# Kernel tuning notes

Measured on AMD Instinct MI355X. Metric: run time of the kernel, lower is better.

## Reference

```python
import jax, jax.numpy as jnp
import numpy as np

N = 50000
IN_CH = 256
HID = 256
E = 800000


def setup_inputs() -> dict:
    key = jax.random.key(0)
    ks = jax.random.split(key, 12)
    s = 1.0 / np.sqrt(HID)
    return {
        "x": jax.random.normal(ks[0], (N, IN_CH), jnp.float32),
        "edge_index": jax.random.randint(ks[1], (2, E), 0, N, dtype=jnp.int64),
        "prev_embedding": jax.random.normal(ks[2], (N, HID), jnp.float32),
        "W1": jax.random.normal(ks[3], (IN_CH, HID), jnp.float32) / np.sqrt(IN_CH),
        "b1": jnp.zeros((HID,), jnp.float32),
        "W2": jax.random.normal(ks[4], (HID, HID), jnp.float32) * s,
        "b2": jnp.zeros((HID,), jnp.float32),
        "gWw": jax.random.normal(ks[5], (HID, HID), jnp.float32) * s,
        "gWb": jnp.zeros((HID,), jnp.float32),
        "gUw": jax.random.normal(ks[6], (HID, HID), jnp.float32) * s,
        "gUb": jnp.zeros((HID,), jnp.float32),
    }


def _gcn_conv(x, W, b, src, dst, norm):
    # PyG GCNConv: h = x @ W; out[i] = sum_j norm_ij * h[j]; + bias
    h = x @ W
    msg = h[src] * norm[:, None]  # [E+N, H]
    out = jax.ops.segment_sum(msg, dst, num_segments=N)
    return out + b


def _norm_and_loops(edge_index):
    loop = jnp.arange(N, dtype=edge_index.dtype)
    src = jnp.concatenate([edge_index[0], loop])
    dst = jnp.concatenate([edge_index[1], loop])
    deg = jax.ops.segment_sum(jnp.ones_like(dst, dtype=jnp.float32), dst, num_segments=N)
    dinv = jnp.where(deg > 0, jax.lax.rsqrt(deg), 0.0)
    norm = dinv[src] * dinv[dst]
    return src, dst, norm


def reference(x, edge_index, prev_embedding, W1, b1, W2, b2, gWw, gWb, gUw, gUb):
    src, dst, norm = _norm_and_loops(edge_index)
    h = jax.nn.relu(_gcn_conv(x, W1, b1, src, dst, norm))
    h_t = _gcn_conv(h, W2, b2, src, dst, norm)
    alpha = jax.nn.sigmoid(h_t @ gWw + gWb + prev_embedding @ gUw + gUb)
    h_tilde = alpha * h_t + (1.0 - alpha) * prev_embedding
    return (h_tilde, h_t)
```

## Files before the change

### kernel.cpp

```cpp
#include <hip/hip_runtime.h>
#include <hip/hip_bf16.h>
#include <math.h>

#define HIDC 256
#define LSTR 40

typedef short short8 __attribute__((ext_vector_type(8)));
typedef float f32x4 __attribute__((ext_vector_type(4)));

__device__ __forceinline__ ushort f2bf_rne(float f) {
    uint u = __float_as_uint(f);
    u += 0x7FFF + ((u >> 16) & 1);
    return (ushort)(u >> 16);
}
__device__ __forceinline__ float bf2f(ushort h) {
    return __uint_as_float(((uint)h) << 16);
}


__global__ void fill_i_kernel(int* __restrict__ p, int v, int n) {
    int i = blockIdx.x * 256 + threadIdx.x;
    if (i < n) p[i] = v;
}

__global__ void deg_kernel(const int* __restrict__ dst, int* __restrict__ deg, int E) {
    int e = blockIdx.x * 256 + threadIdx.x;
    if (e < E) atomicAdd(&deg[dst[e]], 1);
}


__device__ __forceinline__ int block_incl_scan(int v, int tid) {
#pragma unroll
    for (int off = 1; off < 64; off <<= 1) {
        int t = __shfl_up(v, off);
        if ((tid & 63) >= off) v += t;
    }
    __shared__ int wt[4];
    if ((tid & 63) == 63) wt[tid >> 6] = v;
    __syncthreads();
    int wid = tid >> 6;
    for (int w = 0; w < wid; w++) v += wt[w];
    __syncthreads();
    return v;
}

__global__ void scan_a_kernel(const int* __restrict__ deg, int* __restrict__ row_start,
                              int* __restrict__ blocksum, float* __restrict__ dinv, int N) {
    int tid = threadIdx.x;
    int i = blockIdx.x * 256 + tid;
    int v = (i < N) ? deg[i] : 0;
    int incl = block_incl_scan(v, tid);
    if (i < N) {
        row_start[i + 1] = incl;
        dinv[i] = rsqrtf((float)(v + 1));
    }
    if (tid == 255) blocksum[blockIdx.x] = incl;
}

__global__ void scan_b_kernel(int* __restrict__ blocksum, int nb) {
    int tid = threadIdx.x;
    int v = (tid < nb) ? blocksum[tid] : 0;
    int incl = block_incl_scan(v, tid);
    if (tid < nb) blocksum[tid] = incl;
}

__global__ void scan_c_kernel(int* __restrict__ row_start, int* __restrict__ cursor,
                              const int* __restrict__ blocksum, int N) {
    int b = blockIdx.x;
    int i = b * 256 + threadIdx.x;
    int add = (b > 0) ? blocksum[b - 1] : 0;
    if (i < N) {
        int v = row_start[i + 1] + add;
        row_start[i + 1] = v;
        cursor[i + 1] = v;
    }
    if (b == 0 && threadIdx.x == 0) { row_start[0] = 0; cursor[0] = 0; }
}

__global__ void scatter_kernel(const int* __restrict__ src, const int* __restrict__ dst,
                               const float* __restrict__ dinv, int* __restrict__ cursor,
                               int* __restrict__ csr_src, float* __restrict__ csr_w, int E) {
    int e = blockIdx.x * 256 + threadIdx.x;
    if (e < E) {
        int s = src[e], d = dst[e];
        int pos = atomicAdd(&cursor[d], 1);
        csr_src[pos] = s;
        csr_w[pos] = dinv[s] * dinv[d];
    }
}


__global__ void prep_all_kernel(const float* __restrict__ W1, const float* __restrict__ W2,
                                const float* __restrict__ gWw, const float* __restrict__ gUw,
                                ushort* __restrict__ Bt1, ushort* __restrict__ Bt2,
                                ushort* __restrict__ Bth, ushort* __restrict__ Btl) {
    int n = blockIdx.x, k = threadIdx.x;
    Bt1[n * 256 + k] = f2bf_rne(W1[k * 256 + n]);
    Bt2[n * 256 + k] = f2bf_rne(W2[k * 256 + n]);
    float v1 = gWw[k * 256 + n];
    uint u1 = __float_as_uint(v1);
    Bth[n * 512 + k] = (ushort)(u1 >> 16);
    Btl[n * 512 + k] = f2bf_rne(v1 - __uint_as_float(u1 & 0xFFFF0000u));
    float v2 = gUw[k * 256 + n];
    uint u2 = __float_as_uint(v2);
    Bth[n * 512 + 256 + k] = (ushort)(u2 >> 16);
    Btl[n * 512 + 256 + k] = f2bf_rne(v2 - __uint_as_float(u2 & 0xFFFF0000u));
}


__global__ __launch_bounds__(256, 4) void gemm_bf16_kernel(
    const float* __restrict__ A, const ushort* __restrict__ Bt,
    ushort* __restrict__ C, int M)
{
    __shared__ __align__(16) ushort As[128 * LSTR];
    __shared__ __align__(16) ushort Bs[128 * LSTR];
    const int tl = threadIdx.x;
    const int lane = tl & 63, wave = tl >> 6;
    const int wm = (wave & 1) * 64, wn = (wave >> 1) * 64;
    const int bm = blockIdx.x * 128, bn = blockIdx.y * 128;

    const int ar  = tl >> 1;
    const int akq = (tl & 1) * 16;
    const bool aok = (bm + ar) < M;

    f32x4 acc[4][4] = {};

    for (int k0 = 0; k0 < 256; k0 += 32) {
        {
            const float* ap = A + (size_t)(bm + ar) * HIDC + k0 + akq;
#pragma unroll
            for (int j = 0; j < 4; j++) {
                float4 v = aok ? *(const float4*)(ap + 4 * j) : make_float4(0.f, 0.f, 0.f, 0.f);
                ushort4 h;
                h.x = f2bf_rne(v.x); h.y = f2bf_rne(v.y);
                h.z = f2bf_rne(v.z); h.w = f2bf_rne(v.w);
                *(ushort4*)&As[ar * LSTR + akq + 4 * j] = h;
            }
        }
        {
            const ushort* bp = Bt + (size_t)(bn + ar) * 256 + k0 + akq;
            *(uint4*)&Bs[ar * LSTR + akq]     = *(const uint4*)bp;
            *(uint4*)&Bs[ar * LSTR + akq + 8] = *(const uint4*)(bp + 8);
        }
        __syncthreads();
        const int fr = lane & 15, koff = (lane >> 4) * 8;
        short8 af[4], bfv[4];
#pragma unroll
        for (int t = 0; t < 4; t++) {
            af[t]  = *(const short8*)&As[(wm + t * 16 + fr) * LSTR + koff];
            bfv[t] = *(const short8*)&Bs[(wn + t * 16 + fr) * LSTR + koff];
        }
#pragma unroll
        for (int mt = 0; mt < 4; mt++)
#pragma unroll
            for (int nt = 0; nt < 4; nt++)
                acc[mt][nt] = __builtin_amdgcn_mfma_f32_16x16x32_bf16(af[mt], bfv[nt], acc[mt][nt], 0, 0, 0);
        __syncthreads();
    }

    const int row4 = (lane >> 4) * 4, coln = lane & 15;
#pragma unroll
    for (int mt = 0; mt < 4; mt++)
#pragma unroll
        for (int r = 0; r < 4; r++) {
            int m = bm + wm + mt * 16 + row4 + r;
            if (m < M) {
#pragma unroll
                for (int nt = 0; nt < 4; nt++) {
                    int n = bn + wn + nt * 16 + coln;
                    C[(size_t)m * HIDC + n] = f2bf_rne(acc[mt][nt][r]);
                }
            }
        }
}


__global__ __launch_bounds__(256, 4) void gemm_bf16A_kernel(
    const ushort* __restrict__ A, const ushort* __restrict__ Bt,
    ushort* __restrict__ C, int M)
{
    __shared__ __align__(16) ushort As[128 * LSTR];
    __shared__ __align__(16) ushort Bs[128 * LSTR];
    const int tl = threadIdx.x;
    const int lane = tl & 63, wave = tl >> 6;
    const int wm = (wave & 1) * 64, wn = (wave >> 1) * 64;
    const int bm = blockIdx.x * 128, bn = blockIdx.y * 128;

    const int ar  = tl >> 1;
    const int akq = (tl & 1) * 16;
    const bool aok = (bm + ar) < M;

    f32x4 acc[4][4] = {};

    for (int k0 = 0; k0 < 256; k0 += 32) {
        {
            const ushort* ap = A + (size_t)(bm + ar) * HIDC + k0 + akq;
            uint4 z = make_uint4(0u, 0u, 0u, 0u);
            *(uint4*)&As[ar * LSTR + akq]     = aok ? *(const uint4*)ap       : z;
            *(uint4*)&As[ar * LSTR + akq + 8] = aok ? *(const uint4*)(ap + 8) : z;
        }
        {
            const ushort* bp = Bt + (size_t)(bn + ar) * 256 + k0 + akq;
            *(uint4*)&Bs[ar * LSTR + akq]     = *(const uint4*)bp;
            *(uint4*)&Bs[ar * LSTR + akq + 8] = *(const uint4*)(bp + 8);
        }
        __syncthreads();
        const int fr = lane & 15, koff = (lane >> 4) * 8;
        short8 af[4], bfv[4];
#pragma unroll
        for (int t = 0; t < 4; t++) {
            af[t]  = *(const short8*)&As[(wm + t * 16 + fr) * LSTR + koff];
            bfv[t] = *(const short8*)&Bs[(wn + t * 16 + fr) * LSTR + koff];
        }
#pragma unroll
        for (int mt = 0; mt < 4; mt++)
#pragma unroll
            for (int nt = 0; nt < 4; nt++)
                acc[mt][nt] = __builtin_amdgcn_mfma_f32_16x16x32_bf16(af[mt], bfv[nt], acc[mt][nt], 0, 0, 0);
        __syncthreads();
    }

    const int row4 = (lane >> 4) * 4, coln = lane & 15;
#pragma unroll
    for (int mt = 0; mt < 4; mt++)
#pragma unroll
        for (int r = 0; r < 4; r++) {
            int m = bm + wm + mt * 16 + row4 + r;
            if (m < M) {
#pragma unroll
                for (int nt = 0; nt < 4; nt++) {
                    int n = bn + wn + nt * 16 + coln;
                    C[(size_t)m * HIDC + n] = f2bf_rne(acc[mt][nt][r]);
                }
            }
        }
}


__global__ __launch_bounds__(256, 4) void gate_kernel(
    const float* __restrict__ ht, const float* __restrict__ prev,
    const ushort* __restrict__ Bth, const ushort* __restrict__ Btl,
    const float* __restrict__ gWb, const float* __restrict__ gUb,
    float* __restrict__ out, int M)
{
    __shared__ __align__(16) ushort Ash[64 * LSTR];
    __shared__ __align__(16) ushort Asl[64 * LSTR];
    __shared__ __align__(16) ushort Bsh[128 * LSTR];
    __shared__ __align__(16) ushort Bsl[128 * LSTR];
    const int tl = threadIdx.x;
    const int lane = tl & 63, wave = tl >> 6;
    const int wm = (wave & 1) * 32, wn = (wave >> 1) * 64;
    const int bm = blockIdx.x * 64, bn = blockIdx.y * 128;

    const int arA = tl >> 2;
    const int kqA = (tl & 3) * 8;
    const int arB = tl >> 1;
    const int kqB = (tl & 1) * 16;
    const bool aok = (bm + arA) < M;

    f32x4 acc[2][4] = {};

    for (int k0 = 0; k0 < 512; k0 += 32) {
        {
            const float* srcA = (k0 < 256) ? ht : prev;
            const float* ap = srcA + (size_t)(bm + arA) * HIDC + (k0 & 255) + kqA;
            float4 v0 = aok ? *(const float4*)(ap)     : make_float4(0.f, 0.f, 0.f, 0.f);
            float4 v1 = aok ? *(const float4*)(ap + 4) : make_float4(0.f, 0.f, 0.f, 0.f);
            float vv[8] = {v0.x, v0.y, v0.z, v0.w, v1.x, v1.y, v1.z, v1.w};
            ushort hp[8], lp[8];
#pragma unroll
            for (int q = 0; q < 8; q++) {
                uint u = __float_as_uint(vv[q]);
                hp[q] = (ushort)(u >> 16);
                lp[q] = f2bf_rne(vv[q] - __uint_as_float(u & 0xFFFF0000u));
            }
            *(ushort4*)&Ash[arA * LSTR + kqA]     = make_ushort4(hp[0], hp[1], hp[2], hp[3]);
            *(ushort4*)&Ash[arA * LSTR + kqA + 4] = make_ushort4(hp[4], hp[5], hp[6], hp[7]);
            *(ushort4*)&Asl[arA * LSTR + kqA]     = make_ushort4(lp[0], lp[1], lp[2], lp[3]);
            *(ushort4*)&Asl[arA * LSTR + kqA + 4] = make_ushort4(lp[4], lp[5], lp[6], lp[7]);
        }
        {
            const ushort* bph = Bth + (size_t)(bn + arB) * 512 + k0 + kqB;
            const ushort* bpl = Btl + (size_t)(bn + arB) * 512 + k0 + kqB;
            *(uint4*)&Bsh[arB * LSTR + kqB]     = *(const uint4*)bph;
            *(uint4*)&Bsh[arB * LSTR + kqB + 8] = *(const uint4*)(bph + 8);
            *(uint4*)&Bsl[arB * LSTR + kqB]     = *(const uint4*)bpl;
            *(uint4*)&Bsl[arB * LSTR + kqB + 8] = *(const uint4*)(bpl + 8);
        }
        __syncthreads();
        const int fr = lane & 15, koff = (lane >> 4) * 8;
        short8 afh[2], afl[2], bfh[4], bfl[4];
#pragma unroll
        for (int t = 0; t < 2; t++) {
            afh[t] = *(const short8*)&Ash[(wm + t * 16 + fr) * LSTR + koff];
            afl[t] = *(const short8*)&Asl[(wm + t * 16 + fr) * LSTR + koff];
        }
#pragma unroll
        for (int t = 0; t < 4; t++) {
            bfh[t] = *(const short8*)&Bsh[(wn + t * 16 + fr) * LSTR + koff];
            bfl[t] = *(const short8*)&Bsl[(wn + t * 16 + fr) * LSTR + koff];
        }
#pragma unroll
        for (int mt = 0; mt < 2; mt++)
#pragma unroll
            for (int nt = 0; nt < 4; nt++) {
                acc[mt][nt] = __builtin_amdgcn_mfma_f32_16x16x32_bf16(afh[mt], bfh[nt], acc[mt][nt], 0, 0, 0);
                acc[mt][nt] = __builtin_amdgcn_mfma_f32_16x16x32_bf16(afh[mt], bfl[nt], acc[mt][nt], 0, 0, 0);
                acc[mt][nt] = __builtin_amdgcn_mfma_f32_16x16x32_bf16(afl[mt], bfh[nt], acc[mt][nt], 0, 0, 0);
            }
        __syncthreads();
    }

    const int row4 = (lane >> 4) * 4, coln = lane & 15;
#pragma unroll
    for (int mt = 0; mt < 2; mt++)
#pragma unroll
        for (int r = 0; r < 4; r++) {
            int m = bm + wm + mt * 16 + row4 + r;
            if (m < M) {
#pragma unroll
                for (int nt = 0; nt < 4; nt++) {
                    int n = bn + wn + nt * 16 + coln;
                    size_t idx = (size_t)m * HIDC + n;
                    float g = acc[mt][nt][r] + gWb[n] + gUb[n];
                    float alpha = 1.f / (1.f + expf(-g));
                    out[idx] = alpha * ht[idx] + (1.f - alpha) * prev[idx];
                }
            }
        }
}


__global__ __launch_bounds__(256) void csr_agg_kernel(
    const ushort* __restrict__ hm, const int* __restrict__ row_start,
    const int* __restrict__ csr_src, const float* __restrict__ csr_w,
    const float* __restrict__ dinv, const float* __restrict__ bias,
    float* __restrict__ outf, ushort* __restrict__ outb, int do_relu, int N)
{
    const int wave = threadIdx.x >> 6, lane = threadIdx.x & 63;
    const int i = blockIdx.x * 4 + wave;
    if (i >= N) return;
    const int c = lane * 4;

    const float di = dinv[i];
    const float s2 = di * di;
    ushort4 sv = *(const ushort4*)(hm + (size_t)i * HIDC + c);
    float a0 = s2 * bf2f(sv.x), a1 = s2 * bf2f(sv.y);
    float a2 = s2 * bf2f(sv.z), a3 = s2 * bf2f(sv.w);

    const int b0 = row_start[i], b1 = row_start[i + 1];
    int t = b0;
    for (; t + 8 <= b1; t += 8) {
        int   ix[8]; float wv[8]; ushort4 vv[8];
#pragma unroll
        for (int q = 0; q < 8; q++) { ix[q] = csr_src[t + q]; wv[q] = csr_w[t + q]; }
#pragma unroll
        for (int q = 0; q < 8; q++) vv[q] = *(const ushort4*)(hm + (size_t)ix[q] * HIDC + c);
#pragma unroll
        for (int q = 0; q < 8; q++) {
            a0 += wv[q] * bf2f(vv[q].x); a1 += wv[q] * bf2f(vv[q].y);
            a2 += wv[q] * bf2f(vv[q].z); a3 += wv[q] * bf2f(vv[q].w);
        }
    }
    for (; t + 4 <= b1; t += 4) {
        int   i0 = csr_src[t],     i1 = csr_src[t + 1];
        int   i2 = csr_src[t + 2], i3 = csr_src[t + 3];
        float w0 = csr_w[t],       w1 = csr_w[t + 1];
        float w2 = csr_w[t + 2],   w3 = csr_w[t + 3];
        ushort4 v0 = *(const ushort4*)(hm + (size_t)i0 * HIDC + c);
        ushort4 v1 = *(const ushort4*)(hm + (size_t)i1 * HIDC + c);
        ushort4 v2 = *(const ushort4*)(hm + (size_t)i2 * HIDC + c);
        ushort4 v3 = *(const ushort4*)(hm + (size_t)i3 * HIDC + c);
        a0 += w0 * bf2f(v0.x); a1 += w0 * bf2f(v0.y); a2 += w0 * bf2f(v0.z); a3 += w0 * bf2f(v0.w);
        a0 += w1 * bf2f(v1.x); a1 += w1 * bf2f(v1.y); a2 += w1 * bf2f(v1.z); a3 += w1 * bf2f(v1.w);
        a0 += w2 * bf2f(v2.x); a1 += w2 * bf2f(v2.y); a2 += w2 * bf2f(v2.z); a3 += w2 * bf2f(v2.w);
        a0 += w3 * bf2f(v3.x); a1 += w3 * bf2f(v3.y); a2 += w3 * bf2f(v3.z); a3 += w3 * bf2f(v3.w);
    }
    for (; t < b1; ++t) {
        int s_ = csr_src[t];
        float w = csr_w[t];
        ushort4 v = *(const ushort4*)(hm + (size_t)s_ * HIDC + c);
        a0 += w * bf2f(v.x); a1 += w * bf2f(v.y); a2 += w * bf2f(v.z); a3 += w * bf2f(v.w);
    }

    float4 bb = *(const float4*)(bias + c);
    a0 += bb.x; a1 += bb.y; a2 += bb.z; a3 += bb.w;
    if (do_relu) {
        a0 = fmaxf(a0, 0.f); a1 = fmaxf(a1, 0.f);
        a2 = fmaxf(a2, 0.f); a3 = fmaxf(a3, 0.f);
    }
    if (outb) {
        ushort4 o;
        o.x = f2bf_rne(a0); o.y = f2bf_rne(a1);
        o.z = f2bf_rne(a2); o.w = f2bf_rne(a3);
        *(ushort4*)(outb + (size_t)i * HIDC + c) = o;
    } else {
        *(float4*)(outf + (size_t)i * HIDC + c) = make_float4(a0, a1, a2, a3);
    }
}


extern "C" void kernel_launch(void* const* d_in, const int* in_sizes, int n_in,
                              void* d_out, int out_size, void* d_ws, size_t ws_size,
                              hipStream_t stream) {
    const float* x    = (const float*)d_in[0];
    const int*   ei   = (const int*)d_in[1];
    const float* prev = (const float*)d_in[2];
    const float* W1   = (const float*)d_in[3];
    const float* b1   = (const float*)d_in[4];
    const float* W2   = (const float*)d_in[5];
    const float* b2   = (const float*)d_in[6];
    const float* gWw  = (const float*)d_in[7];
    const float* gWb  = (const float*)d_in[8];
    const float* gUw  = (const float*)d_in[9];
    const float* gUb  = (const float*)d_in[10];

    const int N = in_sizes[0] / HIDC;
    const int E = in_sizes[1] / 2;
    const int* src = ei;
    const int* dst = ei + E;

    float* out  = (float*)d_out;
    float* out1 = out;
    float* ht   = out + (size_t)N * HIDC;
    ushort* hbf = (ushort*)out1;

    float* ws = (float*)d_ws;
    size_t o = 0;
    auto take = [&](size_t n) { size_t r = o; o += (n + 63) & ~(size_t)63; return r; };
    float*  dinv    = ws + take(N);
    int*    degi    = (int*)(ws + take(N));
    int*    row_st  = (int*)(ws + take(N + 1));
    int*    cursor  = (int*)(ws + take(N + 1));
    int*    csr_src = (int*)(ws + take(E));
    float*  csr_w   = ws + take(E);
    ushort* Bt1     = (ushort*)(ws + take(256 * 256 / 2));
    ushort* Bt2     = (ushort*)(ws + take(256 * 256 / 2));
    ushort* Bth     = (ushort*)(ws + take(256 * 512 / 2));
    ushort* Btl     = (ushort*)(ws + take(256 * 512 / 2));
    ushort* hm      = (ushort*)(ws + take((size_t)N * HIDC / 2));

    const int nbN = (N + 255) / 256;
    const int nbE = (E + 255) / 256;
    dim3 ggrid((N + 127) / 128, 2);
    dim3 ggridG((N + 63) / 64, 2);
    const int nbAgg = (N + 3) / 4;

    int* blocksum = (int*)csr_w;
    fill_i_kernel<<<nbN, 256, 0, stream>>>(degi, 0, N);
    deg_kernel<<<nbE, 256, 0, stream>>>(dst, degi, E);
    scan_a_kernel<<<nbN, 256, 0, stream>>>(degi, row_st, blocksum, dinv, N);
    scan_b_kernel<<<1, 256, 0, stream>>>(blocksum, nbN);
    scan_c_kernel<<<nbN, 256, 0, stream>>>(row_st, cursor, blocksum, N);
    scatter_kernel<<<nbE, 256, 0, stream>>>(src, dst, dinv, cursor, csr_src, csr_w, E);

    prep_all_kernel<<<256, 256, 0, stream>>>(W1, W2, gWw, gUw, Bt1, Bt2, Bth, Btl);

    gemm_bf16_kernel<<<ggrid, 256, 0, stream>>>(x, Bt1, hm, N);
    csr_agg_kernel<<<nbAgg, 256, 0, stream>>>(hm, row_st, csr_src, csr_w, dinv, b1,
                                              nullptr, hbf, 1, N);

    gemm_bf16A_kernel<<<ggrid, 256, 0, stream>>>(hbf, Bt2, hm, N);
    csr_agg_kernel<<<nbAgg, 256, 0, stream>>>(hm, row_st, csr_src, csr_w, dinv, b2,
                                              ht, nullptr, 0, N);

    gate_kernel<<<ggridG, 256, 0, stream>>>(ht, prev, Bth, Btl, gWb, gUb, out1, N);

    (void)n_in; (void)out_size; (void)ws_size;
}
```

Baseline: 507.1 us.

## Widen gate GEMM tile to full 256 columns so A tile is converted once

The gate kernel now computes all 256 output columns per block instead of splitting N across two grid blocks. Each row block's fp32 A data (h_t and prev) is loaded and split into bf16 hi/lo only once rather than twice. The cost is doubled B shared memory, doubled accumulators and lowered launch bounds occupancy (4 to 3), with half as many blocks in the grid.

```diff
diff --git a/kernel.cpp b/kernel.cpp
--- a/kernel.cpp
+++ b/kernel.cpp
@@ -237,7 +237,7 @@
 }
 
 
-__global__ __launch_bounds__(256, 4) void gate_kernel(
+__global__ __launch_bounds__(256, 3) void gate_kernel(
     const float* __restrict__ ht, const float* __restrict__ prev,
     const ushort* __restrict__ Bth, const ushort* __restrict__ Btl,
     const float* __restrict__ gWb, const float* __restrict__ gUb,
@@ -245,12 +245,12 @@
 {
     __shared__ __align__(16) ushort Ash[64 * LSTR];
     __shared__ __align__(16) ushort Asl[64 * LSTR];
-    __shared__ __align__(16) ushort Bsh[128 * LSTR];
-    __shared__ __align__(16) ushort Bsl[128 * LSTR];
+    __shared__ __align__(16) ushort Bsh[256 * LSTR];
+    __shared__ __align__(16) ushort Bsl[256 * LSTR];
     const int tl = threadIdx.x;
     const int lane = tl & 63, wave = tl >> 6;
-    const int wm = (wave & 1) * 32, wn = (wave >> 1) * 64;
-    const int bm = blockIdx.x * 64, bn = blockIdx.y * 128;
+    const int wm = (wave & 1) * 32, wn = (wave >> 1) * 128;
+    const int bm = blockIdx.x * 64;
 
     const int arA = tl >> 2;
     const int kqA = (tl & 3) * 8;
@@ -258,7 +258,7 @@
     const int kqB = (tl & 1) * 16;
     const bool aok = (bm + arA) < M;
 
-    f32x4 acc[2][4] = {};
+    f32x4 acc[2][8] = {};
 
     for (int k0 = 0; k0 < 512; k0 += 32) {
         {
@@ -280,34 +280,44 @@
             *(ushort4*)&Asl[arA * LSTR + kqA + 4] = make_ushort4(lp[4], lp[5], lp[6], lp[7]);
         }
         {
-            const ushort* bph = Bth + (size_t)(bn + arB) * 512 + k0 + kqB;
-            const ushort* bpl = Btl + (size_t)(bn + arB) * 512 + k0 + kqB;
-            *(uint4*)&Bsh[arB * LSTR + kqB]     = *(const uint4*)bph;
-            *(uint4*)&Bsh[arB * LSTR + kqB + 8] = *(const uint4*)(bph + 8);
-            *(uint4*)&Bsl[arB * LSTR + kqB]     = *(const uint4*)bpl;
-            *(uint4*)&Bsl[arB * LSTR + kqB + 8] = *(const uint4*)(bpl + 8);
+#pragma unroll
+            for (int h = 0; h < 2; h++) {
+                int rB = h * 128 + arB;
+                const ushort* bph = Bth + (size_t)rB * 512 + k0 + kqB;
+                const ushort* bpl = Btl + (size_t)rB * 512 + k0 + kqB;
+                *(uint4*)&Bsh[rB * LSTR + kqB]     = *(const uint4*)bph;
+                *(uint4*)&Bsh[rB * LSTR + kqB + 8] = *(const uint4*)(bph + 8);
+                *(uint4*)&Bsl[rB * LSTR + kqB]     = *(const uint4*)bpl;
+                *(uint4*)&Bsl[rB * LSTR + kqB + 8] = *(const uint4*)(bpl + 8);
+            }
         }
         __syncthreads();
         const int fr = lane & 15, koff = (lane >> 4) * 8;
-        short8 afh[2], afl[2], bfh[4], bfl[4];
+        short8 afh[2], afl[2];
 #pragma unroll
         for (int t = 0; t < 2; t++) {
             afh[t] = *(const short8*)&Ash[(wm + t * 16 + fr) * LSTR + koff];
             afl[t] = *(const short8*)&Asl[(wm + t * 16 + fr) * LSTR + koff];
         }
 #pragma unroll
-        for (int t = 0; t < 4; t++) {
-            bfh[t] = *(const short8*)&Bsh[(wn + t * 16 + fr) * LSTR + koff];
-            bfl[t] = *(const short8*)&Bsl[(wn + t * 16 + fr) * LSTR + koff];
-        }
-#pragma unroll
-        for (int mt = 0; mt < 2; mt++)
-#pragma unroll
-            for (int nt = 0; nt < 4; nt++) {
-                acc[mt][nt] = __builtin_amdgcn_mfma_f32_16x16x32_bf16(afh[mt], bfh[nt], acc[mt][nt], 0, 0, 0);
-                acc[mt][nt] = __builtin_amdgcn_mfma_f32_16x16x32_bf16(afh[mt], bfl[nt], acc[mt][nt], 0, 0, 0);
-                acc[mt][nt] = __builtin_amdgcn_mfma_f32_16x16x32_bf16(afl[mt], bfh[nt], acc[mt][nt], 0, 0, 0);
-            }
+        for (int half = 0; half < 2; half++) {
+            short8 bfh[4], bfl[4];
+#pragma unroll
+            for (int t = 0; t < 4; t++) {
+                int nrow = wn + (half * 4 + t) * 16 + fr;
+                bfh[t] = *(const short8*)&Bsh[nrow * LSTR + koff];
+                bfl[t] = *(const short8*)&Bsl[nrow * LSTR + koff];
+            }
+#pragma unroll
+            for (int mt = 0; mt < 2; mt++)
+#pragma unroll
+                for (int t = 0; t < 4; t++) {
+                    int nt = half * 4 + t;
+                    acc[mt][nt] = __builtin_amdgcn_mfma_f32_16x16x32_bf16(afh[mt], bfh[t], acc[mt][nt], 0, 0, 0);
+                    acc[mt][nt] = __builtin_amdgcn_mfma_f32_16x16x32_bf16(afh[mt], bfl[t], acc[mt][nt], 0, 0, 0);
+                    acc[mt][nt] = __builtin_amdgcn_mfma_f32_16x16x32_bf16(afl[mt], bfh[t], acc[mt][nt], 0, 0, 0);
+                }
+        }
         __syncthreads();
     }
 
@@ -319,8 +329,8 @@
             int m = bm + wm + mt * 16 + row4 + r;
             if (m < M) {
 #pragma unroll
-                for (int nt = 0; nt < 4; nt++) {
-                    int n = bn + wn + nt * 16 + coln;
+                for (int nt = 0; nt < 8; nt++) {
+                    int n = wn + nt * 16 + coln;
                     size_t idx = (size_t)m * HIDC + n;
                     float g = acc[mt][nt][r] + gWb[n] + gUb[n];
                     float alpha = 1.f / (1.f + expf(-g));
@@ -443,7 +453,7 @@
     const int nbN = (N + 255) / 256;
     const int nbE = (E + 255) / 256;
     dim3 ggrid((N + 127) / 128, 2);
-    dim3 ggridG((N + 63) / 64, 2);
+    dim3 ggridG((N + 63) / 64, 1);
     const int nbAgg = (N + 3) / 4;
 
     int* blocksum = (int*)csr_w;
```

Measured after the change: 526.9 us. 1.04x slower.
